# Kernel tuning notes

Hardware: AMD Instinct MI355X
Metric: run time of the kernel (lower is better)

The kernel has to match this reference:

```python
import jax, jax.numpy as jnp
import numpy as np

DK = 128  # key/query head dim (also value dim)

def setup_inputs() -> dict:
    key = jax.random.key(0)
    k1, k2, k3, k4 = jax.random.split(key, 4)
    query = jax.random.normal(k1, (8, 512, 28, 28), dtype=jnp.float32)
    support = jax.random.normal(k2, (16, 512, 28, 28), dtype=jnp.float32)
    Wk = jax.random.normal(k3, (128, 512), dtype=jnp.float32) * (1.0 / np.sqrt(512.0))
    Wv = jax.random.normal(k4, (128, 512), dtype=jnp.float32) * (1.0 / np.sqrt(512.0))
    return {"query": query, "support": support, "Wk": Wk, "Wv": Wv}

def reference(query, support, Wk, Wv):
    B, D, H, W = query.shape
    N, Ds, Hs, Ws = support.shape
    q_flat = query.reshape(B, D, H * W)        # b d u
    s_flat = support.reshape(N, Ds, Hs * Ws)   # n d v
    # 1x1 convs == channel projections (query_head is aliased to key_head)
    q = jnp.einsum('kd,bdu->bku', Wk, q_flat)            # B dk u
    query_value = jnp.einsum('kd,bdu->bku', Wv, q_flat)  # B dv u
    support_key = jnp.einsum('kd,ndv->nkv', Wk, s_flat)  # N dk v
    support_value = jnp.einsum('kd,ndv->nkv', Wv, s_flat)  # N dv v
    scores = jnp.einsum('bku,nkv->bnuv', q, support_key) / jnp.sqrt(jnp.float32(DK))
    # first softmax over dim=3 in the source is dead code (overwritten); effective
    # attention is softmax over the support-class axis n (dim=1)
    attn = jax.nn.softmax(scores, axis=1)  # B N u v
    # note: u is summed out here, exactly as in the source einsum
    query_aligned = jnp.einsum('bnuv,nkv->bkv', attn, support_value)  # B dv v
    a = query_aligned.transpose(0, 2, 1)   # B v dv
    b = query_value.transpose(0, 2, 1)     # B u dv
    # cdist(p=2)**2 == squared euclidean distances; compute without forming diffs
    a2 = jnp.sum(a * a, axis=-1)  # B v
    b2 = jnp.sum(b * b, axis=-1)  # B u
    ab = jnp.einsum('bpd,brd->bpr', a, b)  # B v u
    d2 = jnp.maximum(a2[:, :, None] + b2[:, None, :] - 2.0 * ab, 0.0)
    P, R = d2.shape[1], d2.shape[2]
    return jnp.sum(d2, axis=(1, 2)) / (P * R)  # (B,)
```

## Files before the change

kernel.cpp:

```cpp
#include <hip/hip_runtime.h>

#define U_CNT 784
#define DKH   128
#define DD    512
#define NS    16

typedef short bf16x8 __attribute__((ext_vector_type(8)));
typedef float f32x4  __attribute__((ext_vector_type(4)));

__device__ __forceinline__ unsigned short f2bf(float f) {
  unsigned u = __builtin_bit_cast(unsigned, f);
  u += 0x7fffu + ((u >> 16) & 1u);
  return (unsigned short)(u >> 16);
}


__global__ void cast_w(const float* __restrict__ Wk, const float* __restrict__ Wv,
                       unsigned short* __restrict__ Wkv) {
  int base = (blockIdx.x * 256 + threadIdx.x) * 8;
#pragma unroll
  for (int i = 0; i < 8; ++i) {
    int e = base + i;
    int ko = e >> 9, d = e & 511;
    float v = (ko < 128) ? Wk[ko * 512 + d] : Wv[(ko - 128) * 512 + d];
    Wkv[e] = f2bf(v);
  }
}

__global__ __launch_bounds__(256, 1)
void proj_kernel(const float* __restrict__ query, const float* __restrict__ support,
                 const unsigned short* __restrict__ Wkv,
                 unsigned short* __restrict__ q_f, unsigned short* __restrict__ sk_f,
                 float* __restrict__ sv_t, float* __restrict__ S1p, float* __restrict__ S2p) {
  constexpr int PB = 112;
  constexpr int DR = 128;
  constexpr int ROWW = DR + 4;
  __shared__ float xs[2][PB * ROWW];
  int pc = blockIdx.x;
  int m  = blockIdx.y;
  int tid = threadIdx.x;
  int p0 = pc * PB;
  const float* X = (m < 8) ? (query + (size_t)m * DD * U_CNT)
                           : (support + (size_t)(m - 8) * DD * U_CNT);
  int drow = tid >> 1, pg = tid & 1;
  const float* xrow = X + p0 + pg * 56;

  float4 vbuf[14];
  auto loadR = [&](int rd) {
    const float* s = xrow + (size_t)(rd * DR + drow) * U_CNT;
#pragma unroll
    for (int i = 0; i < 14; ++i) vbuf[i] = *(const float4*)(s + i * 4);
  };
  auto storeR = [&](int bb) {
    float* d0 = &xs[bb][(pg * 56) * ROWW + drow];
#pragma unroll
    for (int i = 0; i < 14; ++i) {
      float* dp = d0 + (i * 4) * ROWW;
      dp[0] = vbuf[i].x; dp[ROWW] = vbuf[i].y;
      dp[2 * ROWW] = vbuf[i].z; dp[3 * ROWW] = vbuf[i].w;
    }
  };

  int wave = tid >> 6, l = tid & 63;
  int col = l & 15, rowg = l >> 4;

  f32x4 acc[7][4];
  f32x4 zero = {0.f, 0.f, 0.f, 0.f};
#pragma unroll
  for (int v7 = 0; v7 < 7; ++v7)
#pragma unroll
    for (int rr = 0; rr < 4; ++rr) acc[v7][rr] = zero;

  loadR(0); storeR(0);
  __syncthreads();
  for (int rd = 0; rd < 4; ++rd) {
    if (rd < 3) loadR(rd + 1);
    int bb = rd & 1;
#pragma unroll
    for (int ds = 0; ds < 4; ++ds) {
      int dl = ds * 32 + rowg * 8;
      bf16x8 Af[4];
#pragma unroll
      for (int rr = 0; rr < 4; ++rr)
        Af[rr] = *(const bf16x8*)(Wkv + (size_t)((wave * 4 + rr) * 16 + col) * DD + rd * DR + dl);
#pragma unroll
      for (int v7 = 0; v7 < 7; ++v7) {
        const float* xp = &xs[bb][(v7 * 16 + col) * ROWW + dl];
        float4 xa = *(const float4*)(xp);
        float4 xb = *(const float4*)(xp + 4);
        bf16x8 bf;
        bf[0] = (short)f2bf(xa.x); bf[1] = (short)f2bf(xa.y);
        bf[2] = (short)f2bf(xa.z); bf[3] = (short)f2bf(xa.w);
        bf[4] = (short)f2bf(xb.x); bf[5] = (short)f2bf(xb.y);
        bf[6] = (short)f2bf(xb.z); bf[7] = (short)f2bf(xb.w);
#pragma unroll
        for (int rr = 0; rr < 4; ++rr)
          acc[v7][rr] = __builtin_amdgcn_mfma_f32_16x16x32_bf16(Af[rr], bf, acc[v7][rr], 0, 0, 0);
      }
    }
    if (rd < 3) {
      __syncthreads();
      storeR((rd + 1) & 1);
      __syncthreads();
    }
  }

  if (m < 8) {
    if (wave < 2) {
#pragma unroll
      for (int rr = 0; rr < 4; ++rr) {
        int r = wave * 4 + rr;
        const float sc = 0.08838834764831845f;
#pragma unroll
        for (int v7 = 0; v7 < 7; ++v7) {
          ushort4 o;
          o.x = f2bf(acc[v7][rr][0] * sc); o.y = f2bf(acc[v7][rr][1] * sc);
          o.z = f2bf(acc[v7][rr][2] * sc); o.w = f2bf(acc[v7][rr][3] * sc);
          size_t off = (size_t)m * 100352 + (size_t)(pc * 7 + v7) * 2048 +
                       (size_t)(2 * r + (rowg >> 1)) * 128 + col * 8 + (rowg & 1) * 4;
          *(ushort4*)(q_f + off) = o;
        }
      }
    } else {
      float s1 = 0.f;
#pragma unroll
      for (int rr = 0; rr < 4; ++rr) {
        int r = wave * 4 + rr;
#pragma unroll
        for (int j = 0; j < 4; ++j) {
          float xsum = 0.f;
#pragma unroll
          for (int v7 = 0; v7 < 7; ++v7) {
            float x = acc[v7][rr][j];
            s1 += x * x; xsum += x;
          }
          xsum += __shfl_xor(xsum, 1, 64); xsum += __shfl_xor(xsum, 2, 64);
          xsum += __shfl_xor(xsum, 4, 64); xsum += __shfl_xor(xsum, 8, 64);
          if (col == 0)
            S2p[((size_t)pc * 8 + m) * DKH + (r - 8) * 16 + rowg * 4 + j] = xsum;
        }
      }
#pragma unroll
      for (int o = 32; o >= 1; o >>= 1) s1 += __shfl_xor(s1, o, 64);
      if (l == 0) S1p[((wave - 2) * 7 + pc) * 8 + m] = s1;
    }
  } else {
    int img = m - 8;
    if (wave < 2) {
#pragma unroll
      for (int rr = 0; rr < 4; ++rr) {
        int r = wave * 4 + rr;
#pragma unroll
        for (int v7 = 0; v7 < 7; ++v7) {
          ushort4 o;
          o.x = f2bf(acc[v7][rr][0]); o.y = f2bf(acc[v7][rr][1]);
          o.z = f2bf(acc[v7][rr][2]); o.w = f2bf(acc[v7][rr][3]);
          size_t off = (size_t)(p0 + v7 * 16 + col) * 2048 +
                       (size_t)(2 * r + (rowg >> 1)) * 128 + img * 8 + (rowg & 1) * 4;
          *(ushort4*)(sk_f + off) = o;
        }
      }
    } else {
#pragma unroll
      for (int rr = 0; rr < 4; ++rr) {
        int r = wave * 4 + rr;
        int kb = (r - 8) * 16 + rowg * 4;
#pragma unroll
        for (int v7 = 0; v7 < 7; ++v7) {
          int p = p0 + v7 * 16 + col;
          float4 o = make_float4(acc[v7][rr][0], acc[v7][rr][1], acc[v7][rr][2], acc[v7][rr][3]);
          *(float4*)(sv_t + (size_t)(img * U_CNT + p) * DKH + kb) = o;
        }
      }
    }
  }
}

__global__ __launch_bounds__(256, 4)
void score_kernel(const unsigned short* __restrict__ q_f,
                  const unsigned short* __restrict__ sk_f,
                  float* __restrict__ w_part) {
  int bx = blockIdx.x;
  int vb = bx % 49;
  int uc = (bx / 49) & 3;
  int b  = bx / 196;
  int wv = threadIdx.x >> 6;
  int l  = threadIdx.x & 63;
  int col = l & 15, rowg = l >> 4;
  int vbase = vb * 16 + wv * 4;

  bf16x8 A[4][4];
#pragma unroll
  for (int v = 0; v < 4; ++v) {
    const unsigned short* ap = sk_f + (size_t)(vbase + v) * 2048 + rowg * 128 + col * 8;
#pragma unroll
    for (int s = 0; s < 4; ++s) A[v][s] = *(const bf16x8*)(ap + s * 512);
  }

  float wl[4][4];
#pragma unroll
  for (int v = 0; v < 4; ++v)
#pragma unroll
    for (int j = 0; j < 4; ++j) wl[v][j] = 0.f;

  int ut0 = (uc == 0) ? 0 : uc * 12 + 1;
  int cnt = (uc == 0) ? 13 : 12;
  const unsigned short* qb = q_f + (size_t)b * 100352 + rowg * 128 + col * 8;
  f32x4 zero = {0.f, 0.f, 0.f, 0.f};

  const unsigned short* qp0 = qb + (size_t)ut0 * 2048;
  bf16x8 B0 = *(const bf16x8*)(qp0);
  bf16x8 B1 = *(const bf16x8*)(qp0 + 512);
  bf16x8 B2 = *(const bf16x8*)(qp0 + 1024);
  bf16x8 B3 = *(const bf16x8*)(qp0 + 1536);

  for (int it = 0; it < cnt; ++it) {
    int nit = (it + 1 < cnt) ? it + 1 : it;
    const unsigned short* qp = qb + (size_t)(ut0 + nit) * 2048;
    bf16x8 N0 = *(const bf16x8*)(qp);
    bf16x8 N1 = *(const bf16x8*)(qp + 512);
    bf16x8 N2 = *(const bf16x8*)(qp + 1024);
    bf16x8 N3 = *(const bf16x8*)(qp + 1536);

    f32x4 acc[4];
#pragma unroll
    for (int v = 0; v < 4; ++v) acc[v] = zero;
#pragma unroll
    for (int v = 0; v < 4; ++v)
      acc[v] = __builtin_amdgcn_mfma_f32_16x16x32_bf16(A[v][0], B0, acc[v], 0, 0, 0);
#pragma unroll
    for (int v = 0; v < 4; ++v)
      acc[v] = __builtin_amdgcn_mfma_f32_16x16x32_bf16(A[v][1], B1, acc[v], 0, 0, 0);
#pragma unroll
    for (int v = 0; v < 4; ++v)
      acc[v] = __builtin_amdgcn_mfma_f32_16x16x32_bf16(A[v][2], B2, acc[v], 0, 0, 0);
#pragma unroll
    for (int v = 0; v < 4; ++v)
      acc[v] = __builtin_amdgcn_mfma_f32_16x16x32_bf16(A[v][3], B3, acc[v], 0, 0, 0);
#pragma unroll
    for (int v = 0; v < 4; ++v) {
      float e0 = __expf(acc[v][0]), e1 = __expf(acc[v][1]);
      float e2 = __expf(acc[v][2]), e3 = __expf(acc[v][3]);
      float ps = (e0 + e1) + (e2 + e3);
      ps += __shfl_xor(ps, 16, 64);
      ps += __shfl_xor(ps, 32, 64);
      float r = __builtin_amdgcn_rcpf(ps);
      wl[v][0] += e0 * r; wl[v][1] += e1 * r;
      wl[v][2] += e2 * r; wl[v][3] += e3 * r;
    }
    B0 = N0; B1 = N1; B2 = N2; B3 = N3;
  }
#pragma unroll
  for (int v = 0; v < 4; ++v)
#pragma unroll
    for (int j = 0; j < 4; ++j) {
      float x = wl[v][j];
      x += __shfl_xor(x, 1, 64); x += __shfl_xor(x, 2, 64);
      x += __shfl_xor(x, 4, 64); x += __shfl_xor(x, 8, 64);
      wl[v][j] = x;
    }
  __shared__ float wst[4][4][16];
#pragma unroll
  for (int v = 0; v < 4; ++v)
    if (col == v) {
#pragma unroll
      for (int j = 0; j < 4; ++j) wst[wv][v][rowg * 4 + j] = wl[v][j];
    }
  __syncthreads();
  int t = threadIdx.x;
  int vl = t >> 4, c = t & 15;
  w_part[(((size_t)uc * 8 + b) * U_CNT + vb * 16 + vl) * NS + c] =
      wst[vl >> 2][vl & 3][c];
}

__global__ __launch_bounds__(256)
void align_kernel(const float* __restrict__ w_part, const float* __restrict__ sv_t,
                  float* __restrict__ T1p, float* __restrict__ T2p) {
  int vt2 = blockIdx.x;
  int t = threadIdx.x;
  __shared__ float w_sh[2][8][16];
  {
    int vl = t >> 7, b = (t >> 4) & 7, n = t & 15;
    float s = 0.f;
#pragma unroll
    for (int uc = 0; uc < 4; ++uc)
      s += w_part[(((size_t)uc * 8 + b) * U_CNT + vt2 * 2 + vl) * NS + n];
    w_sh[vl][b][n] = s;
  }
  __syncthreads();
  int k = t & 127, vl = t >> 7;
  int v = vt2 * 2 + vl;
  float a[8];
#pragma unroll
  for (int b = 0; b < 8; ++b) a[b] = 0.f;
#pragma unroll
  for (int n = 0; n < NS; ++n) {
    float s = sv_t[((size_t)n * U_CNT + v) * DKH + k];
#pragma unroll
    for (int b = 0; b < 8; ++b) a[b] += w_sh[vl][b][n] * s;
  }
  __shared__ float red[8][128];
  if (vl == 1) {
#pragma unroll
    for (int b = 0; b < 8; ++b) red[b][k] = a[b];
  }
  __syncthreads();
  if (vl == 0) {
#pragma unroll
    for (int b = 0; b < 8; ++b)
      T2p[((size_t)vt2 * 8 + b) * DKH + k] = a[b] + red[b][k];
  }
  __shared__ float sw1[4][8];
#pragma unroll
  for (int b = 0; b < 8; ++b) {
    float x = a[b] * a[b];
#pragma unroll
    for (int o = 32; o >= 1; o >>= 1) x += __shfl_xor(x, o, 64);
    if ((t & 63) == 0) sw1[t >> 6][b] = x;
  }
  __syncthreads();
  if (t < 8) T1p[vt2 * 8 + t] = sw1[0][t] + sw1[1][t] + sw1[2][t] + sw1[3][t];
}

__global__ __launch_bounds__(256)
void reduce_partials(const float* __restrict__ S1p, const float* __restrict__ T1p,
                     const float* __restrict__ S2p, const float* __restrict__ T2p,
                     float* __restrict__ S2, float* __restrict__ T2,
                     float* __restrict__ ST1) {
  __shared__ float smem[264];
  int bx = blockIdx.x, t = threadIdx.x;
  if (bx < 32) {
    int b = bx >> 2, kq = bx & 3;
    int kl = t & 31, g = t >> 5;
    int k = kq * 32 + kl;
    float s = 0.f;
    for (int w = g; w < 392; w += 8)
      s += T2p[((size_t)w * 8 + b) * DKH + k];
    smem[g * 32 + kl] = s;
    __syncthreads();
    if (t < 32) {
      float v = 0.f;
#pragma unroll
      for (int g2 = 0; g2 < 8; ++g2) v += smem[g2 * 32 + t];
      T2[b * DKH + kq * 32 + t] = v;
    }
  } else {
    int b = bx - 32;
    int k = t & 127, h = t >> 7;
    float s = 0.f;
    for (int w = h; w < 7; w += 2)
      s += S2p[((size_t)w * 8 + b) * DKH + k];
    if (h == 1) smem[k] = s;
    __syncthreads();
    if (h == 0) S2[b * DKH + k] = s + smem[k];
    float c = 0.f;
    for (int i = t; i < 14; i += 256)  c += S1p[i * 8 + b];
    for (int i = t; i < 392; i += 256) c += T1p[i * 8 + b];
#pragma unroll
    for (int o = 32; o >= 1; o >>= 1) c += __shfl_xor(c, o, 64);
    if ((t & 63) == 0) smem[256 + (t >> 6)] = c;
    __syncthreads();
    if (t == 0) ST1[b] = smem[256] + smem[257] + smem[258] + smem[259];
  }
}

__global__ void final_kernel(const float* __restrict__ S2, const float* __restrict__ T2,
                             const float* __restrict__ ST1, float* __restrict__ out) {
  int b = blockIdx.x, t = threadIdx.x;
  float p = S2[b * DKH + t] * T2[b * DKH + t];
#pragma unroll
  for (int o = 32; o >= 1; o >>= 1) p += __shfl_xor(p, o, 64);
  __shared__ float s2[2];
  if ((t & 63) == 0) s2[t >> 6] = p;
  __syncthreads();
  if (t == 0)
    out[b] = (784.0f * ST1[b] - 2.0f * (s2[0] + s2[1])) * (1.0f / (784.0f * 784.0f));
}

extern "C" void kernel_launch(void* const* d_in, const int* in_sizes, int n_in,
                              void* d_out, int out_size, void* d_ws, size_t ws_size,
                              hipStream_t stream) {
  const float* query   = (const float*)d_in[0];
  const float* support = (const float*)d_in[1];
  const float* Wk      = (const float*)d_in[2];
  const float* Wv      = (const float*)d_in[3];
  float* out = (float*)d_out;
  char* ws = (char*)d_ws;

  unsigned short* Wkv  = (unsigned short*)(ws + 0);
  unsigned short* q_f  = (unsigned short*)(ws + 262144);
  unsigned short* sk_f = (unsigned short*)(ws + 1867776);
  float*          sv_t = (float*)(ws + 5079040);
  float*          w_part = (float*)(ws + 11501568);
  float*          S1p  = (float*)(ws + 14712832);
  float*          T1p  = (float*)(ws + 14716928);
  float*          S2p  = (float*)(ws + 14733312);
  float*          T2p  = (float*)(ws + 14934016);
  float*          S2   = (float*)(ws + 16539648);
  float*          T2   = (float*)(ws + 16543744);
  float*          ST1  = (float*)(ws + 16547840);
  if (ws_size < (size_t)16548000) return;

  cast_w<<<64, 256, 0, stream>>>(Wk, Wv, Wkv);
  proj_kernel<<<dim3(7, 24), 256, 0, stream>>>(query, support, Wkv, q_f, sk_f, sv_t, S1p, S2p);
  score_kernel<<<1568, 256, 0, stream>>>(q_f, sk_f, w_part);
  align_kernel<<<392, 256, 0, stream>>>(w_part, sv_t, T1p, T2p);
  reduce_partials<<<40, 256, 0, stream>>>(S1p, T1p, S2p, T2p, S2, T2, ST1);
  final_kernel<<<8, 128, 0, stream>>>(S2, T2, ST1, out);
}
```

Baseline: 164.5 us.

## Convert to bf16 at LDS store, reorder score blocks, set MFMA priority, fuse reductions

```diff
diff --git a/kernel.cpp b/kernel.cpp
--- a/kernel.cpp
+++ b/kernel.cpp
@@ -34,8 +34,8 @@
                  float* __restrict__ sv_t, float* __restrict__ S1p, float* __restrict__ S2p) {
   constexpr int PB = 112;
   constexpr int DR = 128;
-  constexpr int ROWW = DR + 4;
-  __shared__ float xs[2][PB * ROWW];
+  constexpr int RW = DR + 8;
+  __shared__ __align__(16) unsigned short xs[2][PB * RW];
   int pc = blockIdx.x;
   int m  = blockIdx.y;
   int tid = threadIdx.x;
@@ -52,12 +52,12 @@
     for (int i = 0; i < 14; ++i) vbuf[i] = *(const float4*)(s + i * 4);
   };
   auto storeR = [&](int bb) {
-    float* d0 = &xs[bb][(pg * 56) * ROWW + drow];
+    unsigned short* d0 = &xs[bb][(pg * 56) * RW + drow];
 #pragma unroll
     for (int i = 0; i < 14; ++i) {
-      float* dp = d0 + (i * 4) * ROWW;
-      dp[0] = vbuf[i].x; dp[ROWW] = vbuf[i].y;
-      dp[2 * ROWW] = vbuf[i].z; dp[3 * ROWW] = vbuf[i].w;
+      unsigned short* dp = d0 + (i * 4) * RW;
+      dp[0]      = f2bf(vbuf[i].x); dp[RW]     = f2bf(vbuf[i].y);
+      dp[2 * RW] = f2bf(vbuf[i].z); dp[3 * RW] = f2bf(vbuf[i].w);
     }
   };
 
@@ -85,14 +85,7 @@
         Af[rr] = *(const bf16x8*)(Wkv + (size_t)((wave * 4 + rr) * 16 + col) * DD + rd * DR + dl);
 #pragma unroll
       for (int v7 = 0; v7 < 7; ++v7) {
-        const float* xp = &xs[bb][(v7 * 16 + col) * ROWW + dl];
-        float4 xa = *(const float4*)(xp);
-        float4 xb = *(const float4*)(xp + 4);
-        bf16x8 bf;
-        bf[0] = (short)f2bf(xa.x); bf[1] = (short)f2bf(xa.y);
-        bf[2] = (short)f2bf(xa.z); bf[3] = (short)f2bf(xa.w);
-        bf[4] = (short)f2bf(xb.x); bf[5] = (short)f2bf(xb.y);
-        bf[6] = (short)f2bf(xb.z); bf[7] = (short)f2bf(xb.w);
+        bf16x8 bf = *(const bf16x8*)(&xs[bb][(v7 * 16 + col) * RW + dl]);
 #pragma unroll
         for (int rr = 0; rr < 4; ++rr)
           acc[v7][rr] = __builtin_amdgcn_mfma_f32_16x16x32_bf16(Af[rr], bf, acc[v7][rr], 0, 0, 0);
@@ -181,9 +174,10 @@
                   const unsigned short* __restrict__ sk_f,
                   float* __restrict__ w_part) {
   int bx = blockIdx.x;
-  int vb = bx % 49;
-  int uc = (bx / 49) & 3;
-  int b  = bx / 196;
+  int b  = bx & 7;
+  int inner = bx >> 3;
+  int uc = inner / 49;
+  int vb = inner - uc * 49;
   int wv = threadIdx.x >> 6;
   int l  = threadIdx.x & 63;
   int col = l & 15, rowg = l >> 4;
@@ -225,6 +219,7 @@
     f32x4 acc[4];
 #pragma unroll
     for (int v = 0; v < 4; ++v) acc[v] = zero;
+    __builtin_amdgcn_s_setprio(1);
 #pragma unroll
     for (int v = 0; v < 4; ++v)
       acc[v] = __builtin_amdgcn_mfma_f32_16x16x32_bf16(A[v][0], B0, acc[v], 0, 0, 0);
@@ -237,6 +232,7 @@
 #pragma unroll
     for (int v = 0; v < 4; ++v)
       acc[v] = __builtin_amdgcn_mfma_f32_16x16x32_bf16(A[v][3], B3, acc[v], 0, 0, 0);
+    __builtin_amdgcn_s_setprio(0);
 #pragma unroll
     for (int v = 0; v < 4; ++v) {
       float e0 = __expf(acc[v][0]), e1 = __expf(acc[v][1]);
@@ -323,58 +319,42 @@
 }
 
 __global__ __launch_bounds__(256)
-void reduce_partials(const float* __restrict__ S1p, const float* __restrict__ T1p,
-                     const float* __restrict__ S2p, const float* __restrict__ T2p,
-                     float* __restrict__ S2, float* __restrict__ T2,
-                     float* __restrict__ ST1) {
-  __shared__ float smem[264];
-  int bx = blockIdx.x, t = threadIdx.x;
-  if (bx < 32) {
-    int b = bx >> 2, kq = bx & 3;
-    int kl = t & 31, g = t >> 5;
-    int k = kq * 32 + kl;
-    float s = 0.f;
-    for (int w = g; w < 392; w += 8)
-      s += T2p[((size_t)w * 8 + b) * DKH + k];
-    smem[g * 32 + kl] = s;
-    __syncthreads();
-    if (t < 32) {
-      float v = 0.f;
-#pragma unroll
-      for (int g2 = 0; g2 < 8; ++g2) v += smem[g2 * 32 + t];
-      T2[b * DKH + kq * 32 + t] = v;
-    }
-  } else {
-    int b = bx - 32;
-    int k = t & 127, h = t >> 7;
-    float s = 0.f;
-    for (int w = h; w < 7; w += 2)
-      s += S2p[((size_t)w * 8 + b) * DKH + k];
-    if (h == 1) smem[k] = s;
-    __syncthreads();
-    if (h == 0) S2[b * DKH + k] = s + smem[k];
-    float c = 0.f;
-    for (int i = t; i < 14; i += 256)  c += S1p[i * 8 + b];
-    for (int i = t; i < 392; i += 256) c += T1p[i * 8 + b];
-#pragma unroll
-    for (int o = 32; o >= 1; o >>= 1) c += __shfl_xor(c, o, 64);
-    if ((t & 63) == 0) smem[256 + (t >> 6)] = c;
-    __syncthreads();
-    if (t == 0) ST1[b] = smem[256] + smem[257] + smem[258] + smem[259];
-  }
-}
-
-__global__ void final_kernel(const float* __restrict__ S2, const float* __restrict__ T2,
-                             const float* __restrict__ ST1, float* __restrict__ out) {
-  int b = blockIdx.x, t = threadIdx.x;
-  float p = S2[b * DKH + t] * T2[b * DKH + t];
-#pragma unroll
-  for (int o = 32; o >= 1; o >>= 1) p += __shfl_xor(p, o, 64);
-  __shared__ float s2[2];
-  if ((t & 63) == 0) s2[t >> 6] = p;
+void reduce_final(const float* __restrict__ S1p, const float* __restrict__ T1p,
+                  const float* __restrict__ S2p, const float* __restrict__ T2p,
+                  float* __restrict__ out) {
+  int b = blockIdx.x;
+  int t = threadIdx.x;
+  int k = t & 127, h = t >> 7;
+  __shared__ float sm[128];
+  __shared__ float rw[4];
+
+  float s = 0.f;
+#pragma unroll 4
+  for (int w = h; w < 392; w += 2)
+    s += T2p[((size_t)w * 8 + b) * DKH + k];
+  if (h) sm[k] = s;
+  __syncthreads();
+  float T2k = (!h) ? (s + sm[k]) : 0.f;
+  __syncthreads();
+
+  float s2 = 0.f;
+  for (int w = h; w < 7; w += 2)
+    s2 += S2p[((size_t)w * 8 + b) * DKH + k];
+  if (h) sm[k] = s2;
+  __syncthreads();
+  float p = (!h) ? (s2 + sm[k]) * T2k : 0.f;
+
+  float c = 0.f;
+  for (int i = t; i < 14; i += 256)  c += S1p[i * 8 + b];
+  for (int i = t; i < 392; i += 256) c += T1p[i * 8 + b];
+
+  float q = 784.0f * c - 2.0f * p;
+#pragma unroll
+  for (int o = 32; o >= 1; o >>= 1) q += __shfl_xor(q, o, 64);
+  if ((t & 63) == 0) rw[t >> 6] = q;
   __syncthreads();
   if (t == 0)
-    out[b] = (784.0f * ST1[b] - 2.0f * (s2[0] + s2[1])) * (1.0f / (784.0f * 784.0f));
+    out[b] = (rw[0] + rw[1] + rw[2] + rw[3]) * (1.0f / (784.0f * 784.0f));
 }
 
 extern "C" void kernel_launch(void* const* d_in, const int* in_sizes, int n_in,
@@ -396,15 +376,11 @@
   float*          T1p  = (float*)(ws + 14716928);
   float*          S2p  = (float*)(ws + 14733312);
   float*          T2p  = (float*)(ws + 14934016);
-  float*          S2   = (float*)(ws + 16539648);
-  float*          T2   = (float*)(ws + 16543744);
-  float*          ST1  = (float*)(ws + 16547840);
-  if (ws_size < (size_t)16548000) return;
+  if (ws_size < (size_t)16539648) return;
 
   cast_w<<<64, 256, 0, stream>>>(Wk, Wv, Wkv);
   proj_kernel<<<dim3(7, 24), 256, 0, stream>>>(query, support, Wkv, q_f, sk_f, sv_t, S1p, S2p);
   score_kernel<<<1568, 256, 0, stream>>>(q_f, sk_f, w_part);
   align_kernel<<<392, 256, 0, stream>>>(w_part, sv_t, T1p, T2p);
-  reduce_partials<<<40, 256, 0, stream>>>(S1p, T1p, S2p, T2p, S2, T2, ST1);
-  final_kernel<<<8, 128, 0, stream>>>(S2, T2, ST1, out);
-}
+  reduce_final<<<8, 256, 0, stream>>>(S1p, T1p, S2p, T2p, out);
+}
```

Result: slower. 169.7 us (+3.1%).

## Stage projection inputs as bf16 in LDS, fold log2e into scale, remap score blocks

Applied to the files above, without the earlier changes.

```diff
diff --git a/kernel.cpp b/kernel.cpp
--- a/kernel.cpp
+++ b/kernel.cpp
@@ -34,8 +34,8 @@
                  float* __restrict__ sv_t, float* __restrict__ S1p, float* __restrict__ S2p) {
   constexpr int PB = 112;
   constexpr int DR = 128;
-  constexpr int ROWW = DR + 4;
-  __shared__ float xs[2][PB * ROWW];
+  constexpr int RW = DR + 8;
+  __shared__ __align__(16) unsigned short xs[2][PB * RW];
   int pc = blockIdx.x;
   int m  = blockIdx.y;
   int tid = threadIdx.x;
@@ -52,12 +52,12 @@
     for (int i = 0; i < 14; ++i) vbuf[i] = *(const float4*)(s + i * 4);
   };
   auto storeR = [&](int bb) {
-    float* d0 = &xs[bb][(pg * 56) * ROWW + drow];
+    unsigned short* d0 = &xs[bb][(pg * 56) * RW + drow];
 #pragma unroll
     for (int i = 0; i < 14; ++i) {
-      float* dp = d0 + (i * 4) * ROWW;
-      dp[0] = vbuf[i].x; dp[ROWW] = vbuf[i].y;
-      dp[2 * ROWW] = vbuf[i].z; dp[3 * ROWW] = vbuf[i].w;
+      unsigned short* dp = d0 + (i * 4) * RW;
+      dp[0]      = f2bf(vbuf[i].x); dp[RW]     = f2bf(vbuf[i].y);
+      dp[2 * RW] = f2bf(vbuf[i].z); dp[3 * RW] = f2bf(vbuf[i].w);
     }
   };
 
@@ -85,14 +85,7 @@
         Af[rr] = *(const bf16x8*)(Wkv + (size_t)((wave * 4 + rr) * 16 + col) * DD + rd * DR + dl);
 #pragma unroll
       for (int v7 = 0; v7 < 7; ++v7) {
-        const float* xp = &xs[bb][(v7 * 16 + col) * ROWW + dl];
-        float4 xa = *(const float4*)(xp);
-        float4 xb = *(const float4*)(xp + 4);
-        bf16x8 bf;
-        bf[0] = (short)f2bf(xa.x); bf[1] = (short)f2bf(xa.y);
-        bf[2] = (short)f2bf(xa.z); bf[3] = (short)f2bf(xa.w);
-        bf[4] = (short)f2bf(xb.x); bf[5] = (short)f2bf(xb.y);
-        bf[6] = (short)f2bf(xb.z); bf[7] = (short)f2bf(xb.w);
+        bf16x8 bf = *(const bf16x8*)(&xs[bb][(v7 * 16 + col) * RW + dl]);
 #pragma unroll
         for (int rr = 0; rr < 4; ++rr)
           acc[v7][rr] = __builtin_amdgcn_mfma_f32_16x16x32_bf16(Af[rr], bf, acc[v7][rr], 0, 0, 0);
@@ -110,7 +103,7 @@
 #pragma unroll
       for (int rr = 0; rr < 4; ++rr) {
         int r = wave * 4 + rr;
-        const float sc = 0.08838834764831845f;
+        const float sc = 0.08838834764831845f * 1.4426950408889634f;
 #pragma unroll
         for (int v7 = 0; v7 < 7; ++v7) {
           ushort4 o;
@@ -176,14 +169,15 @@
   }
 }
 
-__global__ __launch_bounds__(256, 4)
+__global__ __launch_bounds__(256, 3)
 void score_kernel(const unsigned short* __restrict__ q_f,
                   const unsigned short* __restrict__ sk_f,
                   float* __restrict__ w_part) {
   int bx = blockIdx.x;
-  int vb = bx % 49;
-  int uc = (bx / 49) & 3;
-  int b  = bx / 196;
+  int b  = bx & 7;
+  int inner = bx >> 3;
+  int uc = inner / 49;
+  int vb = inner - uc * 49;
   int wv = threadIdx.x >> 6;
   int l  = threadIdx.x & 63;
   int col = l & 15, rowg = l >> 4;
@@ -239,8 +233,8 @@
       acc[v] = __builtin_amdgcn_mfma_f32_16x16x32_bf16(A[v][3], B3, acc[v], 0, 0, 0);
 #pragma unroll
     for (int v = 0; v < 4; ++v) {
-      float e0 = __expf(acc[v][0]), e1 = __expf(acc[v][1]);
-      float e2 = __expf(acc[v][2]), e3 = __expf(acc[v][3]);
+      float e0 = exp2f(acc[v][0]), e1 = exp2f(acc[v][1]);
+      float e2 = exp2f(acc[v][2]), e3 = exp2f(acc[v][3]);
       float ps = (e0 + e1) + (e2 + e3);
       ps += __shfl_xor(ps, 16, 64);
       ps += __shfl_xor(ps, 32, 64);
```

Result: no change. 165.6 us (+0.6%).
